# Optimization experiments

Measured on AMD Instinct MI355X. Metric: run time of the kernel, lower is better.

## Reference

```python
import jax, jax.numpy as jnp
import numpy as np


def setup_inputs() -> dict:
    key = jax.random.key(0)
    k_xyz, k_w1, k_b1, k_w2, k_b2 = jax.random.split(key, 5)
    B, N = 2, 1024
    D_MODEL, N_HEADS = 128, 8
    HID = D_MODEL // 2
    # Kaiming-ish init scale for the tiny MLP weights
    return {
        "xyz": jax.random.normal(k_xyz, (B, 3, N), dtype=jnp.float32),
        "W1": jax.random.normal(k_w1, (3, HID), dtype=jnp.float32) * (1.0 / np.sqrt(3.0)),
        "b1": jax.random.normal(k_b1, (HID,), dtype=jnp.float32) * 0.01,
        "W2": jax.random.normal(k_w2, (HID, N_HEADS), dtype=jnp.float32) * (1.0 / np.sqrt(HID)),
        "b2": jax.random.normal(k_b2, (N_HEADS,), dtype=jnp.float32) * 0.01,
    }


def reference(xyz, W1, b1, W2, b2):
    # xyz: [B, 3, N] -> [B, N, 3]
    pts = jnp.transpose(xyz, (0, 2, 1))
    # pairwise relative positions: rel[b, i, j, :] = pts[b, j] - pts[b, i]
    # (matches xyz.unsqueeze(1) - xyz.unsqueeze(2) in torch)
    rel = pts[:, None, :, :] - pts[:, :, None, :]          # [B, N, N, 3]
    h = jax.nn.relu(jnp.einsum("bijc,ch->bijh", rel, W1) + b1)  # [B, N, N, HID]
    bias = jnp.einsum("bijh,hk->bijk", h, W2) + b2         # [B, N, N, H]
    # permute(0, 3, 1, 2) -> [B, H, N, N]
    return jnp.transpose(bias, (0, 3, 1, 2))
```

## Files before the change

kernel.cpp:

```cpp
#include <hip/hip_runtime.h>

#define HID   64
#define NHD   8
#define IT    16
#define IGRP  4
#define WAVES 8
#define JTW   32
#define JT    (WAVES*JTW)

typedef _Float16 f16x8 __attribute__((ext_vector_type(8)));
typedef float    f32x4 __attribute__((ext_vector_type(4)));

__global__ __launch_bounds__(WAVES * 64, 4) void relposenc_pro(
    const float* __restrict__ xyz, const float* __restrict__ W1,
    const float* __restrict__ b1,  const float* __restrict__ W2,
    const float* __restrict__ b2,  float* __restrict__ out, int N) {

  __shared__ float    sW1b1[4][HID];
  __shared__ float    sW2p[HID][NHD + 1];
  __shared__ float    sB2[NHD];
  __shared__ _Float16 sU[IT][HID];

  const int tid  = threadIdx.x;
  const int wave = tid >> 6;
  const int lane = tid & 63;
  const int col  = lane & 15;
  const int hgrp = lane >> 4;
  const int b    = blockIdx.z;
  const int i0   = blockIdx.y * IT;
  const int j0   = blockIdx.x * JT + wave * JTW;

  const float* xb = xyz + (size_t)b * 3 * N;

  sW2p[tid >> 3][tid & 7] = W2[tid];
  if (tid < 4 * HID) {
    int r = tid >> 6, h = tid & 63;
    sW1b1[r][h] = (r < 3) ? W1[r * HID + h] : b1[h];
  }
  if (tid < NHD) sB2[tid] = b2[tid];
  for (int t = tid; t < IT * HID; t += WAVES * 64) {
    int ii = t >> 6, h = t & 63;
    int i  = i0 + ii;
    float u = fmaf(xb[i], W1[h],
              fmaf(xb[N + i], W1[HID + h],
                   xb[2 * N + i] * W1[2 * HID + h]));
    sU[ii][h] = (_Float16)u;
  }

  __syncthreads();

  f16x8 aLo[2], aHi[2];
  #pragma unroll
  for (int kb = 0; kb < 2; ++kb)
    #pragma unroll
    for (int e = 0; e < 8; ++e) {
      int h = kb * 32 + hgrp * 8 + e;
      aLo[kb][e] = (_Float16)((col < NHD)  ? sW2p[h][col]     : 0.f);
      aHi[kb][e] = (_Float16)((col >= NHD) ? sW2p[h][col - 8] : 0.f);
    }
  const int kbase = (hgrp & 1) << 2;
  float b2v[4];
  #pragma unroll
  for (int r = 0; r < 4; ++r) b2v[r] = sB2[kbase + r];

  f16x8 aj[2][2];
  #pragma unroll
  for (int t = 0; t < 2; ++t) {
    int j = j0 + t * 16 + col;
    float x0 = xb[j], x1 = xb[N + j], x2 = xb[2 * N + j];
    #pragma unroll
    for (int kb = 0; kb < 2; ++kb)
      #pragma unroll
      for (int e = 0; e < 8; ++e) {
        int h = kb * 32 + hgrp * 8 + e;
        float v = fmaf(x0, sW1b1[0][h],
                  fmaf(x1, sW1b1[1][h],
                  fmaf(x2, sW1b1[2][h], sW1b1[3][h])));
        aj[t][kb][e] = (_Float16)v;
      }
  }

  const size_t jj = (size_t)j0 + col + ((size_t)(lane >> 5) << 4);
  const size_t baseOff = ((size_t)(b * NHD + kbase) * N + i0) * N + jj;
  const size_t plane = (size_t)N * N;

  const f16x8 z = {0, 0, 0, 0, 0, 0, 0, 0};

  for (int ig = 0; ig < IT; ig += IGRP) {
    f32x4 vals[IGRP];

    #pragma unroll
    for (int q = 0; q < IGRP; ++q) {
      f16x8 u0 = *(const f16x8*)&sU[ig + q][hgrp * 8];
      f16x8 u1 = *(const f16x8*)&sU[ig + q][32 + hgrp * 8];

      f16x8 d00 = __builtin_elementwise_max(aj[0][0] - u0, z);
      f16x8 d01 = __builtin_elementwise_max(aj[0][1] - u1, z);
      f16x8 d10 = __builtin_elementwise_max(aj[1][0] - u0, z);
      f16x8 d11 = __builtin_elementwise_max(aj[1][1] - u1, z);

      f32x4 cA = {b2v[0], b2v[1], b2v[2], b2v[3]};
      f32x4 cB = {0.f, 0.f, 0.f, 0.f};
      cA = __builtin_amdgcn_mfma_f32_16x16x32_f16(aLo[0], d00, cA, 0, 0, 0);
      cA = __builtin_amdgcn_mfma_f32_16x16x32_f16(aLo[1], d01, cA, 0, 0, 0);
      cB = __builtin_amdgcn_mfma_f32_16x16x32_f16(aHi[0], d10, cB, 0, 0, 0);
      cB = __builtin_amdgcn_mfma_f32_16x16x32_f16(aHi[1], d11, cB, 0, 0, 0);
      vals[q] = cA + cB;
    }

    #pragma unroll
    for (int r = 0; r < 4; ++r) {
      const size_t po = baseOff + (size_t)r * plane + (size_t)ig * N;
      #pragma unroll
      for (int q = 0; q < IGRP; ++q)
        out[po + (size_t)q * N] = vals[q][r];
    }
  }
}

extern "C" void kernel_launch(void* const* d_in, const int* in_sizes, int n_in,
                              void* d_out, int out_size, void* d_ws, size_t ws_size,
                              hipStream_t stream) {
  const float* xyz = (const float*)d_in[0];
  const float* W1  = (const float*)d_in[1];
  const float* b1  = (const float*)d_in[2];
  const float* W2  = (const float*)d_in[3];
  const float* b2  = (const float*)d_in[4];
  float* out = (float*)d_out;

  const long long in0 = in_sizes[0];
  const int N = (int)((3LL * (long long)out_size) / (8LL * in0));
  const int B = (int)(in0 / (3LL * N));

  dim3 grid(N / JT, N / IT, B);
  relposenc_pro<<<grid, WAVES * 64, 0, stream>>>(xyz, W1, b1, W2, b2, out, N);
}
```

Before: 22.76 us.

## Stage MFMA outputs in shared memory and drain full head rows with vector stores

Each wave now computes two 32-column j pairs per i row and writes results into a double-buffered shared-memory tile indexed by head. After a block barrier, each wave drains one head's contiguous 512-float row segment with 16-byte stores instead of scattered 4-byte stores. The tile shape also changes to 8 rows by 512 columns. This targets output store coalescing, at the cost of a __syncthreads per row and 32KB of extra shared memory that may lower occupancy.

```diff
diff --git a/kernel.cpp b/kernel.cpp
--- a/kernel.cpp
+++ b/kernel.cpp
@@ -2,16 +2,15 @@
 
 #define HID   64
 #define NHD   8
-#define IT    16
-#define IGRP  4
+#define IT    8
 #define WAVES 8
-#define JTW   32
-#define JT    (WAVES*JTW)
+#define NPAIR 2
+#define JBLK  512
 
 typedef _Float16 f16x8 __attribute__((ext_vector_type(8)));
 typedef float    f32x4 __attribute__((ext_vector_type(4)));
 
-__global__ __launch_bounds__(WAVES * 64, 4) void relposenc_pro(
+__global__ __launch_bounds__(WAVES * 64, 4) void relposenc_rowdrain(
     const float* __restrict__ xyz, const float* __restrict__ W1,
     const float* __restrict__ b1,  const float* __restrict__ W2,
     const float* __restrict__ b2,  float* __restrict__ out, int N) {
@@ -20,6 +19,7 @@
   __shared__ float    sW2p[HID][NHD + 1];
   __shared__ float    sB2[NHD];
   __shared__ _Float16 sU[IT][HID];
+  __shared__ float    sT[2][NHD][JBLK];
 
   const int tid  = threadIdx.x;
   const int wave = tid >> 6;
@@ -28,7 +28,8 @@
   const int hgrp = lane >> 4;
   const int b    = blockIdx.z;
   const int i0   = blockIdx.y * IT;
-  const int j0   = blockIdx.x * JT + wave * JTW;
+  const int jb0  = blockIdx.x * JBLK;
+  const int jwb  = jb0 + wave * (NPAIR * 32);
 
   const float* xb = xyz + (size_t)b * 3 * N;
 
@@ -38,8 +39,8 @@
     sW1b1[r][h] = (r < 3) ? W1[r * HID + h] : b1[h];
   }
   if (tid < NHD) sB2[tid] = b2[tid];
-  for (int t = tid; t < IT * HID; t += WAVES * 64) {
-    int ii = t >> 6, h = t & 63;
+  {
+    int ii = tid >> 6, h = tid & 63;
     int i  = i0 + ii;
     float u = fmaf(xb[i], W1[h],
               fmaf(xb[N + i], W1[HID + h],
@@ -63,41 +64,41 @@
   #pragma unroll
   for (int r = 0; r < 4; ++r) b2v[r] = sB2[kbase + r];
 
-  f16x8 aj[2][2];
+  f16x8 aj[NPAIR][2][2];
   #pragma unroll
-  for (int t = 0; t < 2; ++t) {
-    int j = j0 + t * 16 + col;
-    float x0 = xb[j], x1 = xb[N + j], x2 = xb[2 * N + j];
+  for (int p = 0; p < NPAIR; ++p)
     #pragma unroll
-    for (int kb = 0; kb < 2; ++kb)
+    for (int t = 0; t < 2; ++t) {
+      int j = jwb + p * 32 + t * 16 + col;
+      float x0 = xb[j], x1 = xb[N + j], x2 = xb[2 * N + j];
       #pragma unroll
-      for (int e = 0; e < 8; ++e) {
-        int h = kb * 32 + hgrp * 8 + e;
-        float v = fmaf(x0, sW1b1[0][h],
-                  fmaf(x1, sW1b1[1][h],
-                  fmaf(x2, sW1b1[2][h], sW1b1[3][h])));
-        aj[t][kb][e] = (_Float16)v;
-      }
-  }
+      for (int kb = 0; kb < 2; ++kb)
+        #pragma unroll
+        for (int e = 0; e < 8; ++e) {
+          int h = kb * 32 + hgrp * 8 + e;
+          float v = fmaf(x0, sW1b1[0][h],
+                    fmaf(x1, sW1b1[1][h],
+                    fmaf(x2, sW1b1[2][h], sW1b1[3][h])));
+          aj[p][t][kb][e] = (_Float16)v;
+        }
+    }
 
-  const size_t jj = (size_t)j0 + col + ((size_t)(lane >> 5) << 4);
-  const size_t baseOff = ((size_t)(b * NHD + kbase) * N + i0) * N + jj;
-  const size_t plane = (size_t)N * N;
-
+  const int jdep = wave * (NPAIR * 32) + col + ((lane >> 5) << 4);
   const f16x8 z = {0, 0, 0, 0, 0, 0, 0, 0};
 
-  for (int ig = 0; ig < IT; ig += IGRP) {
-    f32x4 vals[IGRP];
+  float* drainDst = out + (((size_t)(b * NHD + wave)) * N + i0) * N + jb0;
+
+  int buf = 0;
+  for (int ii = 0; ii < IT; ++ii) {
+    f16x8 u0 = *(const f16x8*)&sU[ii][hgrp * 8];
+    f16x8 u1 = *(const f16x8*)&sU[ii][32 + hgrp * 8];
 
     #pragma unroll
-    for (int q = 0; q < IGRP; ++q) {
-      f16x8 u0 = *(const f16x8*)&sU[ig + q][hgrp * 8];
-      f16x8 u1 = *(const f16x8*)&sU[ig + q][32 + hgrp * 8];
-
-      f16x8 d00 = __builtin_elementwise_max(aj[0][0] - u0, z);
-      f16x8 d01 = __builtin_elementwise_max(aj[0][1] - u1, z);
-      f16x8 d10 = __builtin_elementwise_max(aj[1][0] - u0, z);
-      f16x8 d11 = __builtin_elementwise_max(aj[1][1] - u1, z);
+    for (int p = 0; p < NPAIR; ++p) {
+      f16x8 d00 = __builtin_elementwise_max(aj[p][0][0] - u0, z);
+      f16x8 d01 = __builtin_elementwise_max(aj[p][0][1] - u1, z);
+      f16x8 d10 = __builtin_elementwise_max(aj[p][1][0] - u0, z);
+      f16x8 d11 = __builtin_elementwise_max(aj[p][1][1] - u1, z);
 
       f32x4 cA = {b2v[0], b2v[1], b2v[2], b2v[3]};
       f32x4 cB = {0.f, 0.f, 0.f, 0.f};
@@ -105,16 +106,24 @@
       cA = __builtin_amdgcn_mfma_f32_16x16x32_f16(aLo[1], d01, cA, 0, 0, 0);
       cB = __builtin_amdgcn_mfma_f32_16x16x32_f16(aHi[0], d10, cB, 0, 0, 0);
       cB = __builtin_amdgcn_mfma_f32_16x16x32_f16(aHi[1], d11, cB, 0, 0, 0);
-      vals[q] = cA + cB;
+      f32x4 v = cA + cB;
+
+      #pragma unroll
+      for (int r = 0; r < 4; ++r)
+        sT[buf][kbase + r][p * 32 + jdep] = v[r];
     }
 
-    #pragma unroll
-    for (int r = 0; r < 4; ++r) {
-      const size_t po = baseOff + (size_t)r * plane + (size_t)ig * N;
-      #pragma unroll
-      for (int q = 0; q < IGRP; ++q)
-        out[po + (size_t)q * N] = vals[q][r];
+    __syncthreads();
+
+    {
+      const float* src = &sT[buf][wave][0];
+      float* dst = drainDst + (size_t)ii * N;
+      f32x4 v0 = *(const f32x4*)(src + lane * 4);
+      f32x4 v1 = *(const f32x4*)(src + 256 + lane * 4);
+      *(f32x4*)(dst + lane * 4) = v0;
+      *(f32x4*)(dst + 256 + lane * 4) = v1;
     }
+    buf ^= 1;
   }
 }
 
@@ -132,6 +141,6 @@
   const int N = (int)((3LL * (long long)out_size) / (8LL * in0));
   const int B = (int)(in0 / (3LL * N));
 
-  dim3 grid(N / JT, N / IT, B);
-  relposenc_pro<<<grid, WAVES * 64, 0, stream>>>(xyz, W1, b1, W2, b2, out, N);
+  dim3 grid(N / JBLK, N / IT, B);
+  relposenc_rowdrain<<<grid, WAVES * 64, 0, stream>>>(xyz, W1, b1, W2, b2, out, N);
 }
```

Measured after the change: 28.53 us. +25.3%, slower.
